# Kernel optimization log

Measured on AMD Instinct MI355X. Metric: run time of the kernel, lower is better.

## Reference

```python
import jax, jax.numpy as jnp
import numpy as np

EPS = 1e-10
MARGIN = 0.05
DELTA = 0.1
H = W = 512
N = 8388608


def setup_inputs() -> dict:
    key = jax.random.key(0)
    k1, k2, k3, k4 = jax.random.split(key, 4)
    v_input = jax.random.uniform(k1, (3, H, W), dtype=jnp.float32)
    coords = jax.random.randint(k2, (N, 4), 0, W, dtype=jnp.int32)  # x1,y1,x2,y2
    darker = jax.random.randint(k3, (N,), 0, 3, dtype=jnp.int32)
    weights = jax.random.uniform(k4, (N,), dtype=jnp.float32)
    return {"v_input": v_input, "coords": coords, "darker": darker, "weights": weights}


def reference(v_input, coords, darker, weights):
    # v = sum over channels / 3, then affine remap (exactly as torch code)
    v = jnp.sum(v_input, axis=0) / 3.0
    v = (v * 255.0 + 1.0) / 256.0  # [H, W]

    x1, y1, x2, y2 = coords[:, 0], coords[:, 1], coords[:, 2], coords[:, 3]
    r1 = v[y1, x1]
    r2 = v[y2, x2]
    ratio = r1 / (r2 + EPS)
    ratio_inv = r2 / (r1 + EPS)

    b = 1.0 + DELTA + MARGIN
    inv_b = 1.0 / b
    # darker == 1: penalize if ratio > 1/b
    l1 = jnp.where(ratio > inv_b, (ratio - inv_b) + (b - ratio_inv), 0.0)
    # darker == 2: penalize if ratio < b
    l2 = jnp.where(ratio < b, (b - ratio) + (ratio_inv - inv_b), 0.0)
    # darker == 0 (margin <= delta branch): two-sided hinge around [bl, br]
    br = 1.0 + DELTA - MARGIN
    bl = 1.0 / br
    l0 = jnp.where(
        ratio > br,
        (ratio - br) + (bl - ratio_inv),
        jnp.where(ratio < bl, (bl - ratio) + (ratio_inv - br), 0.0),
    )

    per = jnp.where(darker == 1, l1, jnp.where(darker == 2, l2, l0))
    loss = jnp.sum(weights * per) / np.float32(coords.shape[0])
    return loss
```

## Files before the change

### kernel.cpp

```cpp
#include <hip/hip_runtime.h>

#define HW 512
#define NPIX (HW * HW)
#define LDS_PIX 163840
#define THREADS 1024
#define BLOCKS 512
#define NB 4
#define RNDS 4

#define EPS_F  1e-10f
constexpr double B_d  = 1.0 + 0.1 + 0.05;
constexpr double BR_d = 1.0 + 0.1 - 0.05;
#define B_F    ((float)B_d)
#define INVB_F ((float)(1.0 / B_d))
#define BR_F   ((float)BR_d)
#define BL_F   ((float)(1.0 / BR_d))

typedef __attribute__((ext_vector_type(4))) int ivec4;

__global__ void build_v(const float* __restrict__ vin,
                        unsigned char* __restrict__ vq,
                        float* __restrict__ out) {
    int i = blockIdx.x * blockDim.x + threadIdx.x;
    if (i == 0) *out = 0.0f;
    if (i < NPIX) {
        float s = vin[i] + vin[i + NPIX] + vin[i + 2 * NPIX];
        float m = s * (1.0f / 3.0f);
        vq[i] = (unsigned char)__float2int_rn(m * 255.0f);
    }
}

__device__ __forceinline__ float rcp_fast(float x) {
#if __has_builtin(__builtin_amdgcn_rcpf)
    return __builtin_amdgcn_rcpf(x);
#else
    return 1.0f / x;
#endif
}

__device__ __forceinline__ float per_loss(float r1, float r2, int d) {
    float ratio = r1 * rcp_fast(r2 + EPS_F);
    float rinv  = r2 * rcp_fast(r1 + EPS_F);
    float l1 = (ratio > INVB_F) ? (ratio - INVB_F + (B_F - rinv)) : 0.0f;
    float l2 = (ratio < B_F)    ? (B_F - ratio + (rinv - INVB_F)) : 0.0f;
    float l0 = (ratio > BR_F)   ? (ratio - BR_F + (BL_F - rinv))
             : ((ratio < BL_F)  ? (BL_F - ratio + (rinv - BR_F)) : 0.0f);
    return (d == 1) ? l1 : ((d == 2) ? l2 : l0);
}

template<bool PF>
__device__ __forceinline__ void do_round(
        ivec4 (&cc)[NB], int (&dd)[NB], float (&ww)[NB],
        const unsigned char* lv, const unsigned char* __restrict__ vq,
        const ivec4* __restrict__ coords, const int* __restrict__ darker,
        const float* __restrict__ weights,
        int tid, int T, int pfofs, float& acc)
{
    int i1[NB], i2[NB];
    unsigned q1[NB], q2[NB];
    #pragma unroll
    for (int k = 0; k < NB; ++k) {
        i1[k] = cc[k].y * HW + cc[k].x;
        i2[k] = cc[k].w * HW + cc[k].z;
    }
    #pragma unroll
    for (int k = 0; k < NB; ++k) {
        q1[k] = (i1[k] < LDS_PIX) ? (unsigned)lv[i1[k]] : (unsigned)vq[i1[k]];
        q2[k] = (i2[k] < LDS_PIX) ? (unsigned)lv[i2[k]] : (unsigned)vq[i2[k]];
    }
    if (PF) {
        #pragma unroll
        for (int k = 0; k < NB; ++k)
            cc[k] = __builtin_nontemporal_load(&coords[tid + (pfofs + k) * T]);
    }
    __builtin_amdgcn_sched_barrier(0);
    #pragma unroll
    for (int k = 0; k < NB; ++k) {
        float r1 = (float)(q1[k] + 1) * (1.0f / 256.0f);
        float r2 = (float)(q2[k] + 1) * (1.0f / 256.0f);
        acc += ww[k] * per_loss(r1, r2, dd[k]);
    }
    if (PF) {
        #pragma unroll
        for (int k = 0; k < NB; ++k)
            dd[k] = __builtin_nontemporal_load(&darker[tid + (pfofs + k) * T]);
        #pragma unroll
        for (int k = 0; k < NB; ++k)
            ww[k] = __builtin_nontemporal_load(&weights[tid + (pfofs + k) * T]);
        __builtin_amdgcn_sched_barrier(0);
    }
}

__global__ __launch_bounds__(THREADS, 4) void whdr_kernel(
        const unsigned char* __restrict__ vq,
        const ivec4* __restrict__ coords,
        const int*   __restrict__ darker,
        const float* __restrict__ weights,
        float*       __restrict__ out,
        int n) {
    __shared__ unsigned char lv[LDS_PIX];
    const int tid = blockIdx.x * THREADS + threadIdx.x;
    const int T   = BLOCKS * THREADS;
    float acc = 0.0f;

    if (n == T * NB * RNDS) {
        ivec4 cA[NB], cB[NB];
        int   dA[NB], dB[NB];
        float wA[NB], wB[NB];
        #pragma unroll
        for (int k = 0; k < NB; ++k) cA[k] = __builtin_nontemporal_load(&coords[tid + k * T]);
        #pragma unroll
        for (int k = 0; k < NB; ++k) dA[k] = __builtin_nontemporal_load(&darker[tid + k * T]);
        #pragma unroll
        for (int k = 0; k < NB; ++k) wA[k] = __builtin_nontemporal_load(&weights[tid + k * T]);
        #pragma unroll
        for (int k = 0; k < NB; ++k) cB[k] = __builtin_nontemporal_load(&coords[tid + (NB + k) * T]);
        #pragma unroll
        for (int k = 0; k < NB; ++k) dB[k] = __builtin_nontemporal_load(&darker[tid + (NB + k) * T]);
        #pragma unroll
        for (int k = 0; k < NB; ++k) wB[k] = __builtin_nontemporal_load(&weights[tid + (NB + k) * T]);
        {
            const uint4* s4 = (const uint4*)vq;
            uint4* d4 = (uint4*)lv;
            #pragma unroll
            for (int j = threadIdx.x; j < LDS_PIX / 16; j += THREADS) d4[j] = s4[j];
        }
        __syncthreads();

        do_round<true >(cA, dA, wA, lv, vq, coords, darker, weights, tid, T, 2 * NB, acc);
        do_round<true >(cB, dB, wB, lv, vq, coords, darker, weights, tid, T, 3 * NB, acc);
        do_round<false>(cA, dA, wA, lv, vq, coords, darker, weights, tid, T, 0, acc);
        do_round<false>(cB, dB, wB, lv, vq, coords, darker, weights, tid, T, 0, acc);
    } else {
        {
            const uint4* s4 = (const uint4*)vq;
            uint4* d4 = (uint4*)lv;
            for (int j = threadIdx.x; j < LDS_PIX / 16; j += THREADS) d4[j] = s4[j];
        }
        __syncthreads();
        const int TT = gridDim.x * THREADS;
        for (int i = tid; i < n; i += TT) {
            ivec4 c = coords[i];
            int i1 = c.y * HW + c.x, i2 = c.w * HW + c.z;
            unsigned a = (i1 < LDS_PIX) ? (unsigned)lv[i1] : (unsigned)vq[i1];
            unsigned b = (i2 < LDS_PIX) ? (unsigned)lv[i2] : (unsigned)vq[i2];
            float r1 = (float)(a + 1) * (1.0f / 256.0f);
            float r2 = (float)(b + 1) * (1.0f / 256.0f);
            acc += weights[i] * per_loss(r1, r2, darker[i]);
        }
    }

    #pragma unroll
    for (int off = 32; off > 0; off >>= 1)
        acc += __shfl_down(acc, off, 64);
    __syncthreads();
    float* wsum = (float*)lv;
    int lane = threadIdx.x & 63;
    int wid  = threadIdx.x >> 6;
    if (lane == 0) wsum[wid] = acc;
    __syncthreads();
    if (threadIdx.x == 0) {
        float s = 0.0f;
        #pragma unroll
        for (int i = 0; i < THREADS / 64; ++i) s += wsum[i];
        atomicAdd(out, s / (float)n);
    }
}

extern "C" void kernel_launch(void* const* d_in, const int* in_sizes, int n_in,
                              void* d_out, int out_size, void* d_ws, size_t ws_size,
                              hipStream_t stream) {
    const float* v_input = (const float*)d_in[0];
    const ivec4* coords  = (const ivec4*)d_in[1];
    const int*   darker  = (const int*)d_in[2];
    const float* weights = (const float*)d_in[3];
    float* out = (float*)d_out;
    unsigned char* vq = (unsigned char*)d_ws;
    int n = in_sizes[2];

    build_v<<<(NPIX + 255) / 256, 256, 0, stream>>>(v_input, vq, out);
    whdr_kernel<<<BLOCKS, THREADS, 0, stream>>>(vq, coords, darker, weights, out, n);
}
```

Before: 250.8 us.

## Drop LDS staging of lookup table and use smaller blocks with more rounds

Stops copying the first 160K pixels of the quantized brightness table into shared memory per block. All gathers now go straight to the global byte table, relying on L2/MALL caching of the 256KB table. Blocks shrink to 256 threads, the grid grows to 2048 blocks, and each thread runs 8 prefetching rounds of 2 elements. This removes the per-block 160KB copy and barrier and lifts the LDS occupancy limit. In exchange, the random gathers lose the LDS fast path and become global cache traffic.

```diff
diff --git a/kernel.cpp b/kernel.cpp
--- a/kernel.cpp
+++ b/kernel.cpp
@@ -2,11 +2,10 @@
 
 #define HW 512
 #define NPIX (HW * HW)
-#define LDS_PIX 163840
-#define THREADS 1024
-#define BLOCKS 512
-#define NB 4
-#define RNDS 4
+#define THREADS 256
+#define BLOCKS 2048
+#define NB 2
+#define RNDS 8
 
 #define EPS_F  1e-10f
 constexpr double B_d  = 1.0 + 0.1 + 0.05;
@@ -51,7 +50,7 @@
 template<bool PF>
 __device__ __forceinline__ void do_round(
         ivec4 (&cc)[NB], int (&dd)[NB], float (&ww)[NB],
-        const unsigned char* lv, const unsigned char* __restrict__ vq,
+        const unsigned char* __restrict__ vq,
         const ivec4* __restrict__ coords, const int* __restrict__ darker,
         const float* __restrict__ weights,
         int tid, int T, int pfofs, float& acc)
@@ -65,8 +64,8 @@
     }
     #pragma unroll
     for (int k = 0; k < NB; ++k) {
-        q1[k] = (i1[k] < LDS_PIX) ? (unsigned)lv[i1[k]] : (unsigned)vq[i1[k]];
-        q2[k] = (i2[k] < LDS_PIX) ? (unsigned)lv[i2[k]] : (unsigned)vq[i2[k]];
+        q1[k] = vq[i1[k]];
+        q2[k] = vq[i2[k]];
     }
     if (PF) {
         #pragma unroll
@@ -91,14 +90,13 @@
     }
 }
 
-__global__ __launch_bounds__(THREADS, 4) void whdr_kernel(
+__global__ __launch_bounds__(THREADS, 8) void whdr_kernel(
         const unsigned char* __restrict__ vq,
         const ivec4* __restrict__ coords,
         const int*   __restrict__ darker,
         const float* __restrict__ weights,
         float*       __restrict__ out,
         int n) {
-    __shared__ unsigned char lv[LDS_PIX];
     const int tid = blockIdx.x * THREADS + threadIdx.x;
     const int T   = BLOCKS * THREADS;
     float acc = 0.0f;
@@ -119,31 +117,19 @@
         for (int k = 0; k < NB; ++k) dB[k] = __builtin_nontemporal_load(&darker[tid + (NB + k) * T]);
         #pragma unroll
         for (int k = 0; k < NB; ++k) wB[k] = __builtin_nontemporal_load(&weights[tid + (NB + k) * T]);
-        {
-            const uint4* s4 = (const uint4*)vq;
-            uint4* d4 = (uint4*)lv;
-            #pragma unroll
-            for (int j = threadIdx.x; j < LDS_PIX / 16; j += THREADS) d4[j] = s4[j];
-        }
-        __syncthreads();
 
-        do_round<true >(cA, dA, wA, lv, vq, coords, darker, weights, tid, T, 2 * NB, acc);
-        do_round<true >(cB, dB, wB, lv, vq, coords, darker, weights, tid, T, 3 * NB, acc);
-        do_round<false>(cA, dA, wA, lv, vq, coords, darker, weights, tid, T, 0, acc);
-        do_round<false>(cB, dB, wB, lv, vq, coords, darker, weights, tid, T, 0, acc);
+#define RPF(r, S) do_round<true >(c##S, d##S, w##S, vq, coords, darker, weights, tid, T, (r + 2) * NB, acc)
+#define RNP(S)    do_round<false>(c##S, d##S, w##S, vq, coords, darker, weights, tid, T, 0, acc)
+        RPF(0, A); RPF(1, B); RPF(2, A); RPF(3, B);
+        RPF(4, A); RPF(5, B); RNP(A);    RNP(B);
+#undef RPF
+#undef RNP
     } else {
-        {
-            const uint4* s4 = (const uint4*)vq;
-            uint4* d4 = (uint4*)lv;
-            for (int j = threadIdx.x; j < LDS_PIX / 16; j += THREADS) d4[j] = s4[j];
-        }
-        __syncthreads();
         const int TT = gridDim.x * THREADS;
         for (int i = tid; i < n; i += TT) {
             ivec4 c = coords[i];
-            int i1 = c.y * HW + c.x, i2 = c.w * HW + c.z;
-            unsigned a = (i1 < LDS_PIX) ? (unsigned)lv[i1] : (unsigned)vq[i1];
-            unsigned b = (i2 < LDS_PIX) ? (unsigned)lv[i2] : (unsigned)vq[i2];
+            unsigned a = vq[c.y * HW + c.x];
+            unsigned b = vq[c.w * HW + c.z];
             float r1 = (float)(a + 1) * (1.0f / 256.0f);
             float r2 = (float)(b + 1) * (1.0f / 256.0f);
             acc += weights[i] * per_loss(r1, r2, darker[i]);
@@ -153,8 +139,7 @@
     #pragma unroll
     for (int off = 32; off > 0; off >>= 1)
         acc += __shfl_down(acc, off, 64);
-    __syncthreads();
-    float* wsum = (float*)lv;
+    __shared__ float wsum[THREADS / 64];
     int lane = threadIdx.x & 63;
     int wid  = threadIdx.x >> 6;
     if (lane == 0) wsum[wid] = acc;
```

New measurement: 320.6 us. 1.28x slower.
